# Optimization experiments

Measured on AMD Instinct MI355X. Metric: run time of the kernel, lower is better.

The kernel has to match this reference:

```python
import jax, jax.numpy as jnp
import numpy as np
import math

B, N, D = 2, 192, 256

def _linear_params(key, d_in, d_out):
    kw, kb = jax.random.split(key)
    scale = 1.0 / math.sqrt(d_in)
    W = jax.random.uniform(kw, (d_out, d_in), jnp.float32, -scale, scale)
    b = jax.random.uniform(kb, (d_out,), jnp.float32, -scale, scale)
    return W, b

def setup_inputs() -> dict:
    key = jax.random.key(0)
    ks = jax.random.split(key, 7)
    Edges = jax.random.normal(ks[0], (B, N * N, D), jnp.float32)
    Wq_w, Wq_b = _linear_params(ks[1], D, D)
    Wk_w, Wk_b = _linear_params(ks[2], D, D)
    Wv_w, Wv_b = _linear_params(ks[3], D, D)
    Wb_w, Wb_b = _linear_params(ks[4], D, 1)
    Wg_w, Wg_b = _linear_params(ks[5], D, D)
    Wo_w, Wo_b = _linear_params(ks[6], D, D)
    return {"Edges": Edges, "Wq_w": Wq_w, "Wq_b": Wq_b, "Wk_w": Wk_w, "Wk_b": Wk_b,
            "Wv_w": Wv_w, "Wv_b": Wv_b, "Wb_w": Wb_w, "Wb_b": Wb_b,
            "Wg_w": Wg_w, "Wg_b": Wg_b, "Wo_w": Wo_w, "Wo_b": Wo_b}

def reference(Edges, Wq_w, Wq_b, Wk_w, Wk_b, Wv_w, Wv_b, Wb_w, Wb_b, Wg_w, Wg_b, Wo_w, Wo_b):
    # Edges: [B, N*N, D]; dropout is identity in eval mode.
    Bb, NN, Dd = Edges.shape
    n = int(round(math.sqrt(NN)))
    q = (Edges @ Wq_w.T + Wq_b).reshape(Bb, n, n, Dd)
    k = (Edges @ Wk_w.T + Wk_b).reshape(Bb, n, n, Dd)
    v = (Edges @ Wv_w.T + Wv_b).reshape(Bb, n, n, Dd)
    bmat = (Edges @ Wb_w.T + Wb_b).reshape(Bb, n, n)          # b[b,i,l]
    g = jax.nn.sigmoid(Edges @ Wg_w.T + Wg_b)                  # [B, N*N, D]
    # row attention: q(i,j) . k(i,l) ; column attention: q(i,j) . k(l,j)
    scores = (jnp.einsum('bijd,bild->bijl', q, k)
              + jnp.einsum('bijd,bljd->bijl', q, k)) / math.sqrt(Dd)
    sym_bias = bmat + jnp.swapaxes(bmat, 1, 2)                 # b[i,l] + b[l,i]
    alpha = jax.nn.softmax(scores + sym_bias[:, :, None, :], axis=-1)  # [B,n,n,n]
    # first value contraction along rows; second term matches torch's
    # transpose-free add: out2[b,i,j,d] = sum_l alpha[b,j,i,l] v[b,l,i,d]
    o1 = jnp.einsum('bijl,bild->bijd', alpha, v)
    o2 = jnp.einsum('bjil,blid->bijd', alpha, v)
    out = g * (o1 + o2).reshape(Bb, NN, Dd)
    out = jax.nn.relu(out @ Wo_w.T + Wo_b)
    return out
```

## Files before the change

kernel.cpp:

```cpp
#include <hip/hip_runtime.h>
#include <hip/hip_bf16.h>

typedef __hip_bfloat16 bf16;
typedef unsigned short u16;
typedef __attribute__((ext_vector_type(8))) short bf16x8;
typedef __attribute__((ext_vector_type(4))) float f32x4;

#define NB   2
#define NG   192
#define DD   256
#define NN2  (NG*NG)
#define MT   (NB*NN2)

static __device__ __forceinline__ float bfu2f(u16 u){
    return __uint_as_float(((unsigned)u) << 16);
}
static __device__ __forceinline__ u16 f2bfu(float f){
    bf16 h = __float2bfloat16(f);
    return *(u16*)&h;
}

static __device__ __forceinline__ void gl_lds16(const void* g, void* l){
    __builtin_amdgcn_global_load_lds(
        (const __attribute__((address_space(1))) unsigned int*)g,
        (__attribute__((address_space(3))) unsigned int*)l, 16, 0, 0);
}
static __device__ __forceinline__ int swz3(int x){ return ((x ^ (x>>3)) & 7) << 3; }

__global__ __launch_bounds__(256) void k_cast_eb(
    const float* __restrict__ E, const float* __restrict__ Wb,
    const float* __restrict__ bb, u16* __restrict__ Eb, float* __restrict__ bm)
{
    const int t = threadIdx.x;
    size_t base = (size_t)blockIdx.x*2048 + t*8;
    float4 x = *(const float4*)(E+base);
    float4 y = *(const float4*)(E+base+4);
    ushort4 a; a.x=f2bfu(x.x); a.y=f2bfu(x.y); a.z=f2bfu(x.z); a.w=f2bfu(x.w);
    ushort4 b; b.x=f2bfu(y.x); b.y=f2bfu(y.y); b.z=f2bfu(y.z); b.w=f2bfu(y.w);
    *(ushort4*)(Eb+base)   = a;
    *(ushort4*)(Eb+base+4) = b;
    const int l32 = t & 31;
    float4 w0 = ((const float4*)Wb)[l32*2];
    float4 w1 = ((const float4*)Wb)[l32*2+1];
    float s = x.x*w0.x + x.y*w0.y + x.z*w0.z + x.w*w0.w
            + y.x*w1.x + y.y*w1.y + y.z*w1.z + y.w*w1.w;
    #pragma unroll
    for (int off=1; off<32; off<<=1) s += __shfl_xor(s, off);
    if (l32 == 0) bm[blockIdx.x*8 + (t>>5)] = s + bb[0];
}

__global__ __launch_bounds__(256) void k_cast_w(
    const float* __restrict__ Wq, const float* __restrict__ Wk,
    const float* __restrict__ Wv, const float* __restrict__ Wg,
    const float* __restrict__ Wo,
    const float* __restrict__ bq, const float* __restrict__ bk,
    const float* __restrict__ bv, const float* __restrict__ bg,
    u16* __restrict__ Wcat, u16* __restrict__ Wob, float* __restrict__ biascat)
{
    int e = blockIdx.x*256 + threadIdx.x;
    Wcat[e]          = f2bfu(Wq[e]);
    Wcat[65536 + e]  = f2bfu(Wk[e]);
    Wcat[131072 + e] = f2bfu(Wv[e]);
    Wcat[196608 + e] = f2bfu(Wg[e]);
    Wob[e]           = f2bfu(Wo[e]);
    if (e < 1024){
        int p = e>>8, r = e&255;
        const float* bp = p==0?bq : p==1?bk : p==2?bv : bg;
        biascat[e] = bp[r];
    }
}

__global__ __launch_bounds__(256) void k_bias_sym(
    const float* __restrict__ bm, float* __restrict__ biassym)
{
    int rem = blockIdx.x*256 + threadIdx.x;
    int b = blockIdx.y;
    int i = rem / NG, l = rem % NG;
    biassym[(size_t)b*NN2 + rem] = bm[(size_t)b*NN2 + rem] + bm[(size_t)b*NN2 + l*NG + i];
}

static __device__ __forceinline__ void gemm128_dbuf(
    const u16* __restrict__ A, const u16* __restrict__ B,
    u16* As, u16* Bs, f32x4 acc[4][4], int t)
{
    const int lane = t & 63, w = t >> 6;
    const int wm = (w>>1)*64, wn = (w&1)*64;
    int offA[4], offB[4];
    #pragma unroll
    for (int f=0; f<4; f++){
        int ra = wm + f*16 + (lane&15);
        offA[f] = ra*32 + (((lane>>4) ^ ((ra>>1)&3)) << 3);
        int rb = wn + f*16 + (lane&15);
        offB[f] = rb*32 + (((lane>>4) ^ ((rb>>1)&3)) << 3);
    }
    auto stage = [&](int buf, int k0){
        #pragma unroll
        for (int it=0; it<2; it++){
            int c = it*256 + t;
            int row = c >> 2;
            int ks  = (c&3) ^ ((row>>1)&3);
            gl_lds16(A + (size_t)row*DD + k0 + ks*8, As + buf*4096 + c*8);
            gl_lds16(B + (size_t)row*DD + k0 + ks*8, Bs + buf*4096 + c*8);
        }
    };
    stage(0, 0);
    for (int ks=0; ks<8; ks++){
        if (ks<7){
            stage((ks+1)&1, (ks+1)*32);
            asm volatile("s_waitcnt vmcnt(4)" ::: "memory");
        } else {
            asm volatile("s_waitcnt vmcnt(0)" ::: "memory");
        }
        __builtin_amdgcn_s_barrier();
        const u16* Ab = As + (ks&1)*4096;
        const u16* Bb = Bs + (ks&1)*4096;
        bf16x8 a[4], b[4];
        #pragma unroll
        for (int f=0; f<4; f++) a[f] = *(const bf16x8*)(Ab + offA[f]);
        #pragma unroll
        for (int f=0; f<4; f++) b[f] = *(const bf16x8*)(Bb + offB[f]);
        #pragma unroll
        for (int mf=0; mf<4; mf++)
            #pragma unroll
            for (int nf=0; nf<4; nf++)
                acc[mf][nf] = __builtin_amdgcn_mfma_f32_16x16x32_bf16(a[mf], b[nf], acc[mf][nf], 0, 0, 0);
        __builtin_amdgcn_s_barrier();
    }
}

__global__ __launch_bounds__(256, 2) void k_proj_mfma(
    const u16* __restrict__ Eb, const u16* __restrict__ Wcat,
    const float* __restrict__ biascat,
    u16* __restrict__ qb, u16* __restrict__ kb,
    u16* __restrict__ vb, u16* __restrict__ gb)
{
    __shared__ u16 As[2*4096];
    const int blk = blockIdx.x;
    const int xj = blk & 7, xi = blk >> 3;
    const int m0 = (xj*72 + (xi>>3)) * 128;
    const int n0 = (xi & 7) * 128;
    const int t = threadIdx.x, lane = t&63, w = t>>6;
    const int wm = (w>>1)*64, wn = (w&1)*64;

    bf16x8 bfr[8][4];
    {
        const u16* Wb0 = Wcat + (size_t)(n0 + wn + (lane&15))*DD + (lane>>4)*8;
        #pragma unroll
        for (int f=0; f<4; f++){
            const u16* Wr = Wb0 + (size_t)f*16*DD;
            #pragma unroll
            for (int ks=0; ks<8; ks++)
                bfr[ks][f] = *(const bf16x8*)(Wr + ks*32);
        }
    }

    const u16* A = Eb + (size_t)m0*DD;
    int offA[4];
    #pragma unroll
    for (int f=0; f<4; f++){
        int ra = wm + f*16 + (lane&15);
        offA[f] = ra*32 + (((lane>>4) ^ ((ra>>1)&3)) << 3);
    }
    auto stageA = [&](int buf, int k0){
        #pragma unroll
        for (int it=0; it<2; it++){
            int c = it*256 + t;
            int row = c >> 2;
            int ks  = (c&3) ^ ((row>>1)&3);
            gl_lds16(A + (size_t)row*DD + k0 + ks*8, As + buf*4096 + c*8);
        }
    };

    f32x4 acc[4][4];
    #pragma unroll
    for (int i=0;i<4;i++)
        #pragma unroll
        for (int j=0;j<4;j++) acc[i][j] = f32x4{0.f,0.f,0.f,0.f};

    stageA(0, 0);
    #pragma unroll
    for (int ks=0; ks<8; ks++){
        if (ks<7){
            stageA((ks+1)&1, (ks+1)*32);
            asm volatile("s_waitcnt vmcnt(2)" ::: "memory");
        } else {
            asm volatile("s_waitcnt vmcnt(0)" ::: "memory");
        }
        __builtin_amdgcn_s_barrier();
        const u16* Ab = As + (ks&1)*4096;
        bf16x8 a[4];
        #pragma unroll
        for (int f=0; f<4; f++) a[f] = *(const bf16x8*)(Ab + offA[f]);
        #pragma unroll
        for (int mf=0; mf<4; mf++)
            #pragma unroll
            for (int nf=0; nf<4; nf++)
                acc[mf][nf] = __builtin_amdgcn_mfma_f32_16x16x32_bf16(a[mf], bfr[ks][nf], acc[mf][nf], 0, 0, 0);
        __builtin_amdgcn_s_barrier();
    }

    const int p = n0 >> 8;
    u16* outp = p==0?qb : p==1?kb : p==2?vb : gb;
    #pragma unroll
    for (int mf=0; mf<4; mf++){
        int m = m0 + wm + mf*16 + (lane>>4)*4;
        #pragma unroll
        for (int nf=0; nf<4; nf++){
            int gn = n0 + wn + nf*16 + (lane&15);
            float bias = biascat[gn];
            int col = gn & 255;
            #pragma unroll
            for (int r=0; r<4; r++){
                float v = acc[mf][nf][r] + bias;
                if (p==3) v = 1.0f/(1.0f+__expf(-v));
                outp[(size_t)(m+r)*DD + col] = f2bfu(v);
            }
        }
    }
}

__global__ __launch_bounds__(256) void k_final_mfma(
    const u16* __restrict__ hb, const u16* __restrict__ Wob,
    const float* __restrict__ bo, float* __restrict__ out)
{
    __shared__ u16 As[2*4096];
    __shared__ u16 Bs[2*4096];
    const int blk = blockIdx.x;
    const int xj = blk & 7, xi = blk >> 3;
    const int m0 = (xj*72 + (xi>>1)) * 128;
    const int n0 = (xi & 1) * 128;
    const int t = threadIdx.x, lane = t&63, w = t>>6;
    f32x4 acc[4][4];
    #pragma unroll
    for (int i=0;i<4;i++)
        #pragma unroll
        for (int j=0;j<4;j++) acc[i][j] = f32x4{0.f,0.f,0.f,0.f};
    gemm128_dbuf(hb + (size_t)m0*DD, Wob + (size_t)n0*DD, As, Bs, acc, t);

    const int wm = (w>>1)*64, wn = (w&1)*64;
    #pragma unroll
    for (int mf=0; mf<4; mf++){
        int m = m0 + wm + mf*16 + (lane>>4)*4;
        #pragma unroll
        for (int nf=0; nf<4; nf++){
            int n = n0 + wn + nf*16 + (lane&15);
            float bias = bo[n];
            #pragma unroll
            for (int r=0; r<4; r++)
                out[(size_t)(m+r)*DD + n] = fmaxf(acc[mf][nf][r] + bias, 0.0f);
        }
    }
}

__global__ __launch_bounds__(512, 2) void k_scores(
    const u16* __restrict__ q, const u16* __restrict__ kmat,
    u16* __restrict__ S1, u16* __restrict__ S2T)
{
    __shared__ u16 As[2][NG*64];
    __shared__ u16 Bs[2][NG*64];
    const int MODE = blockIdx.y;
    const int z = blockIdx.x, b = z/NG, r = z%NG;
    const int t = threadIdx.x, lane = t&63, w = t>>6;
    const int wm = (w&3)*48, wn = (w>>2)*96;
    const size_t astr = MODE ? (size_t)NG*DD : (size_t)DD;
    const u16* Ab = MODE ? q    + ((size_t)b*NN2 + r)*DD : q    + ((size_t)b*NG + r)*NG*DD;
    const u16* Bb = MODE ? kmat + ((size_t)b*NN2 + r)*DD : kmat + ((size_t)b*NG + r)*NG*DD;

    f32x4 acc[3][6];
    #pragma unroll
    for (int i=0;i<3;i++)
        #pragma unroll
        for (int j=0;j<6;j++) acc[i][j] = f32x4{0.f,0.f,0.f,0.f};

    int offA[3], offB[6];
    #pragma unroll
    for (int mf=0; mf<3; mf++){
        int x = wm + mf*16 + (lane&15);
        offA[mf] = x*64 + (((lane>>4)<<3) ^ swz3(x));
    }
    #pragma unroll
    for (int nf=0; nf<6; nf++){
        int x = wn + nf*16 + (lane&15);
        offB[nf] = x*64 + (((lane>>4)<<3) ^ swz3(x));
    }

    auto stage = [&](int buf, int k0){
        #pragma unroll
        for (int rr=0; rr<3; rr++){
            int c = t + rr*512;
            int x = c>>3, l8e = (c&7)<<3;
            size_t ro = (size_t)x*astr + k0;
            gl_lds16(Ab + ro + (l8e ^ swz3(x)), &As[buf][c*8]);
            gl_lds16(Bb + ro + (l8e ^ swz3(x)), &Bs[buf][c*8]);
        }
    };

    stage(0, 0);
    for (int ks=0; ks<4; ks++){
        if (ks<3){
            stage((ks+1)&1, (ks+1)*64);
            asm volatile("s_waitcnt vmcnt(6)" ::: "memory");
        } else {
            asm volatile("s_waitcnt vmcnt(0)" ::: "memory");
        }
        __builtin_amdgcn_s_barrier();
        const u16* A = &As[ks&1][0];
        const u16* B = &Bs[ks&1][0];
        #pragma unroll
        for (int kk=0; kk<2; kk++){
            bf16x8 a[3];
            #pragma unroll
            for (int mf=0; mf<3; mf++) a[mf] = *(const bf16x8*)(A + (offA[mf]^(kk<<5)));
            #pragma unroll
            for (int nf=0; nf<6; nf++){
                bf16x8 bf = *(const bf16x8*)(B + (offB[nf]^(kk<<5)));
                #pragma unroll
                for (int mf=0; mf<3; mf++)
                    acc[mf][nf] = __builtin_amdgcn_mfma_f32_16x16x32_bf16(a[mf], bf, acc[mf][nf], 0, 0, 0);
            }
        }
        __builtin_amdgcn_s_barrier();
    }

    u16* outb = (MODE ? S2T : S1) + ((size_t)b*NG + r)*NN2;
    #pragma unroll
    for (int mf=0; mf<3; mf++){
        #pragma unroll
        for (int nf=0; nf<6; nf++){
            int lcol = wn + nf*16 + (lane&15);
            #pragma unroll
            for (int r4=0; r4<4; r4++){
                int x = wm + mf*16 + (lane>>4)*4 + r4;
                outb[(size_t)x*NG + lcol] = f2bfu(acc[mf][nf][r4]*0.0625f);
            }
        }
    }
}

__global__ __launch_bounds__(256) void k_softmax(
    const u16* __restrict__ S1, const u16* __restrict__ S2T,
    const float* __restrict__ biassym,
    u16* __restrict__ alpha, u16* __restrict__ alphaT)
{
    int rr   = blockIdx.x*4 + (threadIdx.x >> 6);
    int lane = threadIdx.x & 63;
    int b = blockIdx.y;
    int i = rr / NG, j = rr % NG;
    const u16* r1 = S1  + ((size_t)b*NN2 + rr)*NG;
    const u16* r2 = S2T + ((size_t)b*NN2 + (size_t)j*NG + i)*NG;
    const float* bs = biassym + ((size_t)b*NG + i)*NG;
    float vals[3];
    float mx = -1e30f;
    #pragma unroll
    for (int tt=0; tt<3; tt++){
        int l = lane + tt*64;
        float s = bfu2f(r1[l]) + bfu2f(r2[l]) + bs[l];
        vals[tt] = s;
        mx = fmaxf(mx, s);
    }
    #pragma unroll
    for (int off=32; off; off>>=1) mx = fmaxf(mx, __shfl_xor(mx, off));
    float sum = 0.f;
    #pragma unroll
    for (int tt=0; tt<3; tt++){ vals[tt] = __expf(vals[tt]-mx); sum += vals[tt]; }
    #pragma unroll
    for (int off=32; off; off>>=1) sum += __shfl_xor(sum, off);
    float inv = 1.0f/sum;
    u16* arow1 = alpha  + ((size_t)b*NN2 + rr)*NG;
    u16* arow2 = alphaT + ((size_t)b*NN2 + (size_t)j*NG + i)*NG;
    #pragma unroll
    for (int tt=0; tt<3; tt++){
        u16 vq = f2bfu(vals[tt]*inv);
        arow1[lane + tt*64] = vq;
        arow2[lane + tt*64] = vq;
    }
}

__global__ __launch_bounds__(512, 4) void k_attnout(
    const u16* __restrict__ alpha, const u16* __restrict__ alphaT,
    const u16* __restrict__ vb, const u16* __restrict__ gb, u16* __restrict__ hb)
{
    __shared__ u16 AsL[2][NG*64];
    __shared__ u16 Vs[128*64];
    const int z = blockIdx.x;
    const int xcd = z & 7, s = z >> 3;
    const int bi = xcd*48 + (s>>1), dh = s & 1;
    const int b = bi/NG, i = bi%NG;
    const int dbase = dh*128;
    const int t = threadIdx.x, lane = t&63, w = t>>6;
    const int wm = (w&1)*96, wn = (w>>1)*32;

    const u16* Abase0 = alpha  + (size_t)bi*NN2;
    const u16* Abase1 = alphaT + (size_t)bi*NN2;
    const u16* V0 = vb + (size_t)bi*NG*DD + dbase;
    const u16* V1 = vb + ((size_t)b*NG*NG + i)*DD + dbase;

    f32x4 acc[6][2];
    #pragma unroll
    for (int m=0;m<6;m++)
        #pragma unroll
        for (int n=0;n<2;n++) acc[m][n] = f32x4{0.f,0.f,0.f,0.f};

    int offA[6], offB[2];
    #pragma unroll
    for (int mf=0; mf<6; mf++){
        int j = wm + mf*16 + (lane&15);
        offA[mf] = j*64 + (((lane>>4)<<3) ^ swz3(j));
    }
    #pragma unroll
    for (int nf=0; nf<2; nf++){
        int d = wn + nf*16 + (lane&15);
        offB[nf] = d*64 + (((lane>>4)<<3) ^ swz3(d));
    }

    int4 vr[2];
    auto stageA = [&](int u, int buf){
        const u16* Ab = (u>=3) ? Abase1 : Abase0;
        int ls = (u>=3 ? u-3 : u)*64;
        #pragma unroll
        for (int rr=0; rr<3; rr++){
            int c = t + rr*512;
            int j = c>>3, l8e = (c&7)<<3;
            gl_lds16(Ab + (size_t)j*NG + ls + (l8e ^ swz3(j)), &AsL[buf][c*8]);
        }
    };
    auto loadV = [&](int u){
        int p = (u>=3), ls = (u>=3 ? u-3 : u)*64;
        #pragma unroll
        for (int rr=0; rr<2; rr++){
            int c = t + rr*512;
            int l = ls + (c>>4), d0 = (c&15)*8;
            const u16* src = p ? (V1 + (size_t)l*NG*DD + d0) : (V0 + (size_t)l*DD + d0);
            vr[rr] = *(const int4*)src;
        }
    };

    stageA(0, 0);
    loadV(0);
    for (int u=0; u<6; u++){
        #pragma unroll
        for (int rr=0; rr<2; rr++){
            int c = t + rr*512;
            int l = c>>4;
            l &= 63;
            int d0 = (c&15)*8, c3 = c&7;
            ushort* vp = (ushort*)&vr[rr];
            #pragma unroll
            for (int qd=0; qd<8; qd++)
                Vs[(d0+qd)*64 + (l ^ ((qd^c3)<<3))] = vp[qd];
        }
        if (u<5){ stageA(u+1, (u+1)&1); loadV(u+1); }
        asm volatile("s_waitcnt lgkmcnt(0)" ::: "memory");
        __builtin_amdgcn_s_barrier();
        const u16* A = &AsL[u&1][0];
        #pragma unroll
        for (int kk=0; kk<2; kk++){
            bf16x8 bfr[2];
            #pragma unroll
            for (int nf=0; nf<2; nf++) bfr[nf] = *(const bf16x8*)(Vs + (offB[nf]^(kk<<5)));
            #pragma unroll
            for (int mf=0; mf<6; mf++){
                bf16x8 afr = *(const bf16x8*)(A + (offA[mf]^(kk<<5)));
                acc[mf][0] = __builtin_amdgcn_mfma_f32_16x16x32_bf16(afr, bfr[0], acc[mf][0], 0, 0, 0);
                acc[mf][1] = __builtin_amdgcn_mfma_f32_16x16x32_bf16(afr, bfr[1], acc[mf][1], 0, 0, 0);
            }
        }
        __builtin_amdgcn_s_barrier();
    }

    #pragma unroll
    for (int mf=0; mf<6; mf++){
        #pragma unroll
        for (int nf=0; nf<2; nf++){
            #pragma unroll
            for (int r4=0; r4<4; r4++){
                int j = wm + mf*16 + (lane>>4)*4 + r4;
                int d = dbase + wn + nf*16 + (lane&15);
                size_t idx = ((size_t)bi*NG + j)*DD + d;
                hb[idx] = f2bfu(bfu2f(gb[idx]) * acc[mf][nf][r4]);
            }
        }
    }
}

extern "C" void kernel_launch(void* const* d_in, const int* in_sizes, int n_in,
                              void* d_out, int out_size, void* d_ws, size_t ws_size,
                              hipStream_t stream)
{
    const float* E  = (const float*)d_in[0];
    const float* Wq = (const float*)d_in[1];  const float* bq = (const float*)d_in[2];
    const float* Wk = (const float*)d_in[3];  const float* bk = (const float*)d_in[4];
    const float* Wv = (const float*)d_in[5];  const float* bv = (const float*)d_in[6];
    const float* Wb = (const float*)d_in[7];  const float* bb = (const float*)d_in[8];
    const float* Wg = (const float*)d_in[9];  const float* bg = (const float*)d_in[10];
    const float* Wo = (const float*)d_in[11]; const float* bo = (const float*)d_in[12];
    float* out = (float*)d_out;

    const size_t BF = (size_t)MT*DD*2;
    const size_t SC = (size_t)NB*NG*NG*NG*4;
    char* ws = (char*)d_ws;
    u16* Eb  = (u16*)ws;
    u16* S1  = (u16*)ws;
    u16* S2T = (u16*)(ws + SC/2);
    u16* hb  = (u16*)ws;
    u16* qb = (u16*)(ws + SC);           u16* alpha  = qb;
    u16* kb = (u16*)(ws + SC + BF);      u16* alphaT = kb;
    u16* vb = (u16*)(ws + SC + 2*BF);
    u16* gb = (u16*)(ws + SC + 3*BF);
    size_t tail = SC + 4*BF;
    float* bm      = (float*)(ws + tail); tail += (size_t)MT*4;
    float* biassym = (float*)(ws + tail); tail += (size_t)MT*4;
    u16* Wcat      = (u16*)(ws + tail);   tail += (size_t)1024*DD*2;
    u16* Wob       = (u16*)(ws + tail);   tail += (size_t)DD*DD*2;
    float* biascat = (float*)(ws + tail); tail += 1024*4;
    (void)ws_size;

    k_cast_w   <<<dim3(256), 256, 0, stream>>>(Wq,Wk,Wv,Wg,Wo, bq,bk,bv,bg, Wcat, Wob, biascat);
    k_cast_eb  <<<dim3(9216), 256, 0, stream>>>(E, Wb, bb, Eb, bm);
    k_proj_mfma<<<dim3(4608), 256, 0, stream>>>(Eb, Wcat, biascat, qb, kb, vb, gb);
    k_bias_sym <<<dim3(NN2/256, NB), 256, 0, stream>>>(bm, biassym);
    k_scores   <<<dim3(NB*NG, 2), 512, 0, stream>>>(qb, kb, S1, S2T);
    k_softmax  <<<dim3(NN2/4, NB), 256, 0, stream>>>(S1, S2T, biassym, alpha, alphaT);
    k_attnout  <<<dim3(NB*NG*2), 512, 0, stream>>>(alpha, alphaT, vb, gb, hb);
    k_final_mfma<<<dim3(1152), 256, 0, stream>>>(hb, Wob, bo, out);
}
```

Baseline: 275.4 us.

## Stream projection weight fragments through a 3-slot register ring instead of preloading all

Result: faster. 263.9 us (-4.2%).

```diff
diff --git a/kernel.cpp b/kernel.cpp
--- a/kernel.cpp
+++ b/kernel.cpp
@@ -128,7 +128,7 @@
     }
 }
 
-__global__ __launch_bounds__(256, 2) void k_proj_mfma(
+__global__ __launch_bounds__(256) void k_proj_mfma(
     const u16* __restrict__ Eb, const u16* __restrict__ Wcat,
     const float* __restrict__ biascat,
     u16* __restrict__ qb, u16* __restrict__ kb,
@@ -142,25 +142,13 @@
     const int t = threadIdx.x, lane = t&63, w = t>>6;
     const int wm = (w>>1)*64, wn = (w&1)*64;
 
-    bf16x8 bfr[8][4];
-    {
-        const u16* Wb0 = Wcat + (size_t)(n0 + wn + (lane&15))*DD + (lane>>4)*8;
-        #pragma unroll
-        for (int f=0; f<4; f++){
-            const u16* Wr = Wb0 + (size_t)f*16*DD;
-            #pragma unroll
-            for (int ks=0; ks<8; ks++)
-                bfr[ks][f] = *(const bf16x8*)(Wr + ks*32);
-        }
-    }
-
-    const u16* A = Eb + (size_t)m0*DD;
     int offA[4];
     #pragma unroll
     for (int f=0; f<4; f++){
         int ra = wm + f*16 + (lane&15);
         offA[f] = ra*32 + (((lane>>4) ^ ((ra>>1)&3)) << 3);
     }
+    const u16* A = Eb + (size_t)m0*DD;
     auto stageA = [&](int buf, int k0){
         #pragma unroll
         for (int it=0; it<2; it++){
@@ -171,6 +159,13 @@
         }
     };
 
+    const u16* Wb0 = Wcat + (size_t)(n0 + wn + (lane&15))*DD + (lane>>4)*8;
+    bf16x8 breg[3][4];
+    #define LOADB(slot, kss) { \
+        _Pragma("unroll") \
+        for (int f=0; f<4; f++) \
+            breg[slot][f] = *(const bf16x8*)(Wb0 + (size_t)f*16*DD + (kss)*32); }
+
     f32x4 acc[4][4];
     #pragma unroll
     for (int i=0;i<4;i++)
@@ -178,26 +173,29 @@
         for (int j=0;j<4;j++) acc[i][j] = f32x4{0.f,0.f,0.f,0.f};
 
     stageA(0, 0);
+    LOADB(0, 0);
+    LOADB(1, 1);
     #pragma unroll
     for (int ks=0; ks<8; ks++){
-        if (ks<7){
-            stageA((ks+1)&1, (ks+1)*32);
-            asm volatile("s_waitcnt vmcnt(2)" ::: "memory");
-        } else {
-            asm volatile("s_waitcnt vmcnt(0)" ::: "memory");
-        }
+        if (ks<7) stageA((ks+1)&1, (ks+1)*32);
+        if (ks<6) { LOADB((ks+2)%3, ks+2); }
+        if (ks<6)      asm volatile("s_waitcnt vmcnt(6)" ::: "memory");
+        else if (ks==6) asm volatile("s_waitcnt vmcnt(2)" ::: "memory");
+        else           asm volatile("s_waitcnt vmcnt(0)" ::: "memory");
         __builtin_amdgcn_s_barrier();
         const u16* Ab = As + (ks&1)*4096;
         bf16x8 a[4];
         #pragma unroll
         for (int f=0; f<4; f++) a[f] = *(const bf16x8*)(Ab + offA[f]);
+        const int s = ks % 3;
         #pragma unroll
         for (int mf=0; mf<4; mf++)
             #pragma unroll
             for (int nf=0; nf<4; nf++)
-                acc[mf][nf] = __builtin_amdgcn_mfma_f32_16x16x32_bf16(a[mf], bfr[ks][nf], acc[mf][nf], 0, 0, 0);
-        __builtin_amdgcn_s_barrier();
-    }
+                acc[mf][nf] = __builtin_amdgcn_mfma_f32_16x16x32_bf16(a[mf], breg[s][nf], acc[mf][nf], 0, 0, 0);
+        __builtin_amdgcn_s_barrier();
+    }
+    #undef LOADB
 
     const int p = n0 >> 8;
     u16* outp = p==0?qb : p==1?kb : p==2?vb : gb;
```
